# Performance work log

Hardware: AMD Instinct MI355X
Metric: run time of the kernel (lower is better)

## Reference

```python
import jax, jax.numpy as jnp
import numpy as np

B, N, D = 4, 8192, 128
H = 4 * D  # exp_factor * features
EPS = 1e-5


def layer_norm(x):
    # fresh nn.LayerNorm each call -> weight=1, bias=0 (no learned affine)
    mu = jnp.mean(x, axis=-1, keepdims=True)
    var = jnp.var(x, axis=-1, keepdims=True)
    return (x - mu) * jax.lax.rsqrt(var + EPS)


def setup_inputs() -> dict:
    key = jax.random.key(0)
    ks = jax.random.split(key, 8)
    x = jax.random.normal(ks[0], (B, N, D), dtype=jnp.float32)
    adj = jax.random.uniform(ks[1], (N, N), dtype=jnp.float32)
    attn_mask = jnp.ones((1,), dtype=jnp.int32)  # unused (torch masked_fill result discarded)
    pad_mask = jnp.ones((1,), dtype=jnp.int32)   # unused
    # FFN params (torch Linear default init scale ~ 1/sqrt(fan_in))
    w1 = jax.random.normal(ks[2], (D, H), dtype=jnp.float32) / np.sqrt(D)
    b1 = jnp.zeros((H,), dtype=jnp.float32)
    w2 = jax.random.normal(ks[3], (H, D), dtype=jnp.float32) / np.sqrt(H)
    b2 = jnp.zeros((D,), dtype=jnp.float32)
    return {"x": x, "adj": adj, "attn_mask": attn_mask, "pad_mask": pad_mask,
            "w1": w1, "b1": b1, "w2": w2, "b2": b2, "dim": 128}


def reference(x, adj, attn_mask, pad_mask, w1, b1, w2, b2, dim):
    # Sublayer 0: x + InrAwaSA(LN(x))
    h = layer_norm(x)                               # [B,N,D]
    # adj is provided -> scores = dense adj, shared across batch.
    # NOTE: masks are no-ops in the source (masked_fill not in-place).
    prob = jax.nn.softmax(adj, axis=-1)             # [N,N]
    attn_out = jnp.einsum('nm,bmd->bnd', prob, h)   # [B,N,D]
    x1 = x + attn_out
    # Sublayer 1: x1 + FFN(LN(x1))
    h1 = layer_norm(x1)
    ffn = jnp.maximum(h1 @ w1 + b1, 0.0) @ w2 + b2
    return x1 + ffn
```

## Files before the change

kernel.cpp:

```cpp
#include <hip/hip_runtime.h>
#include <hip/hip_bf16.h>

typedef __attribute__((ext_vector_type(8))) short bh8;
typedef __attribute__((ext_vector_type(4))) float fx4;
typedef __attribute__((ext_vector_type(8))) int i32x8;
typedef __attribute__((ext_vector_type(4))) int i32x4;

typedef const __attribute__((address_space(1))) unsigned int* gas_p;
typedef __attribute__((address_space(3))) unsigned int* las_p;

#define MFMA(a, b, c) __builtin_amdgcn_mfma_f32_16x16x32_bf16((a), (b), (c), 0, 0, 0)
#define MFMAS(a, b, c) __builtin_amdgcn_mfma_scale_f32_16x16x128_f8f6f4( \
    (a), (b), (c), 0, 0, 0, 0x7f7f7f7f, 0, 0x7f7f7f7f)

__device__ __forceinline__ unsigned short f2bf(float f) {
  unsigned u = __builtin_bit_cast(unsigned, f);
  u += 0x7fff + ((u >> 16) & 1);
  return (unsigned short)(u >> 16);
}

__device__ __forceinline__ float bflo2f(unsigned u) { return __builtin_bit_cast(float, u << 16); }

__device__ __forceinline__ void gld16(const void* g, void* l) {
  __builtin_amdgcn_global_load_lds((gas_p)g, (las_p)l, 16, 0, 0);
}

__global__ __launch_bounds__(256) void transpose_weights(const float* __restrict__ w1,
                                                         const float* __restrict__ w2,
                                                         unsigned short* __restrict__ w1t,
                                                         unsigned short* __restrict__ w2t) {
  const int tgl = blockIdx.x * 256 + threadIdx.x;
  { const int h = tgl >> 7, d = tgl & 127; w1t[tgl] = f2bf(w1[d * 512 + h]); }
  { const int d = tgl >> 9, h = tgl & 511; w2t[tgl] = f2bf(w2[h * 128 + d]); }
}

__global__ __launch_bounds__(256) void ln1_transpose(const float* __restrict__ x,
                                                     unsigned char* __restrict__ htf) {
  const int t = threadIdx.x, lane = t & 63, w = t >> 6;
  const int mt = blockIdx.x, b = blockIdx.y;
  __shared__ unsigned short tile[128 * 64];
  const float* xb = x + ((size_t)b * 8192 + (size_t)mt * 64) * 128;
  for (int it = 0; it < 16; ++it) {
    const int r = w * 16 + it;
    const float2 v = *(const float2*)(xb + r * 128 + lane * 2);
    float s = v.x + v.y, s2 = v.x * v.x + v.y * v.y;
    #pragma unroll
    for (int o = 1; o < 64; o <<= 1) { s += __shfl_xor(s, o); s2 += __shfl_xor(s2, o); }
    const float mean = s * 0.0078125f;
    const float var = s2 * 0.0078125f - mean * mean;
    const float rstd = rsqrtf(var + 1e-5f);
    const int mc = r >> 3, ml = r & 7;
    const int d0 = lane * 2, d1 = d0 + 1;
    tile[d0 * 64 + ((mc ^ (d0 & 7)) << 3) + ml] = f2bf((v.x - mean) * rstd);
    tile[d1 * 64 + ((mc ^ (d1 & 7)) << 3) + ml] = f2bf((v.y - mean) * rstd);
  }
  __syncthreads();
  #pragma unroll
  for (int i = 0; i < 4; ++i) {
    const int idx = i * 256 + t;
    const int d = idx >> 3, mc = idx & 7;
    const bh8 vv = *(const bh8*)(tile + d * 64 + ((mc ^ (d & 7)) << 3));
    int lo = 0, hi = 0;
    lo = __builtin_amdgcn_cvt_pk_fp8_f32(bflo2f((unsigned short)vv[0]),
                                         bflo2f((unsigned short)vv[1]), lo, false);
    lo = __builtin_amdgcn_cvt_pk_fp8_f32(bflo2f((unsigned short)vv[2]),
                                         bflo2f((unsigned short)vv[3]), lo, true);
    hi = __builtin_amdgcn_cvt_pk_fp8_f32(bflo2f((unsigned short)vv[4]),
                                         bflo2f((unsigned short)vv[5]), hi, false);
    hi = __builtin_amdgcn_cvt_pk_fp8_f32(bflo2f((unsigned short)vv[6]),
                                         bflo2f((unsigned short)vv[7]), hi, true);
    const int col = b * 128 + d;
    const int k0 = mt * 64 + mc * 8;
    const int frag = (k0 >> 7) * 32 + (col >> 4);
    const int off = ((col & 15) + 16 * ((k0 >> 5) & 3)) * 32 + (k0 & 31);
    *(uint2*)(htf + (size_t)frag * 2048 + off) = (uint2){(unsigned)lo, (unsigned)hi};
  }
}

__global__ __launch_bounds__(256) void softmax_frag(const float* __restrict__ adj,
                                                    unsigned char* __restrict__ probf) {
  const int t = threadIdx.x, lane = t & 63, w = t >> 6;
  const size_t n = blockIdx.x;
  __shared__ float red[4];
  __shared__ unsigned char sp[8192];
  const fx4* row = (const fx4*)(adj + n * 8192);
  fx4 v[8];
  float lsum = 0.f;
  #pragma unroll
  for (int i = 0; i < 8; ++i) {
    const fx4 a = row[i * 256 + t];
    fx4 e;
    e.x = __expf(a.x); e.y = __expf(a.y); e.z = __expf(a.z); e.w = __expf(a.w);
    v[i] = e;
    lsum += e.x + e.y + e.z + e.w;
  }
  #pragma unroll
  for (int o = 1; o < 64; o <<= 1) lsum += __shfl_xor(lsum, o);
  if (lane == 0) red[w] = lsum;
  __syncthreads();
  const float rinv = 4096.f / (red[0] + red[1] + red[2] + red[3]);
  #pragma unroll
  for (int i = 0; i < 8; ++i) {
    int pk = 0;
    pk = __builtin_amdgcn_cvt_pk_fp8_f32(v[i].x * rinv, v[i].y * rinv, pk, false);
    pk = __builtin_amdgcn_cvt_pk_fp8_f32(v[i].z * rinv, v[i].w * rinv, pk, true);
    const int g = 64 * i + (t >> 2);
    const int pg = g ^ ((g >> 4) & 7);
    *(unsigned*)&sp[pg * 16 + (t & 3) * 4] = (unsigned)pk;
  }
  __syncthreads();
  const int g0 = 2 * t, g1 = 2 * t + 1;
  const i32x4 q0 = *(const i32x4*)&sp[(g0 ^ ((g0 >> 4) & 7)) * 16];
  const i32x4 q1 = *(const i32x4*)&sp[(g1 ^ ((g1 >> 4) & 7)) * 16];
  unsigned char* dst = probf + (((n >> 4) * 64 + (t >> 2)) * 2048)
                     + (((int)(n & 15) + 16 * (t & 3)) * 32);
  *(i32x4*)dst = q0;
  *(i32x4*)(dst + 16) = q1;
}

__global__ __launch_bounds__(256, 2) void attn_gemm(const unsigned char* __restrict__ probf,
                                                    const unsigned char* __restrict__ htf,
                                                    unsigned short* __restrict__ pbuf) {
  const int tid = threadIdx.x, lane = tid & 63, wn = tid >> 6;
  const int mt = blockIdx.x, z = blockIdx.y;

  fx4 acc[4][8];
  #pragma unroll
  for (int i = 0; i < 4; ++i)
    #pragma unroll
    for (int j = 0; j < 8; ++j) acc[i][j] = (fx4){0.f, 0.f, 0.f, 0.f};

  for (int tt = 0; tt < 16; ++tt) {
    const int gkt = z * 16 + tt;
    i32x8 afr[4];
    #pragma unroll
    for (int mf = 0; mf < 4; ++mf) {
      const unsigned char* ap =
          probf + ((size_t)((mt * 4 + mf) * 64 + gkt)) * 2048 + lane * 32;
      const i32x4 lo = *(const i32x4*)ap;
      const i32x4 hi = *(const i32x4*)(ap + 16);
      afr[mf] = (i32x8){lo.x, lo.y, lo.z, lo.w, hi.x, hi.y, hi.z, hi.w};
    }
    const unsigned char* fb = htf + ((size_t)gkt * 32 + wn * 8) * 2048 + lane * 32;
    #pragma unroll
    for (int nf = 0; nf < 8; ++nf) {
      const i32x4 blo = *(const i32x4*)(fb + nf * 2048);
      const i32x4 bhi = *(const i32x4*)(fb + nf * 2048 + 16);
      const i32x8 bfr = (i32x8){blo.x, blo.y, blo.z, blo.w, bhi.x, bhi.y, bhi.z, bhi.w};
      #pragma unroll
      for (int mf = 0; mf < 4; ++mf)
        acc[mf][nf] = MFMAS(afr[mf], bfr, acc[mf][nf]);
    }
  }

  const float ds = 0.000244140625f;
  unsigned short* po = pbuf + (size_t)z * 8192 * 512;
  #pragma unroll
  for (int mf = 0; mf < 4; ++mf)
    #pragma unroll
    for (int nf = 0; nf < 8; ++nf) {
      const int col = wn * 128 + nf * 16 + (lane & 15);
      #pragma unroll
      for (int q = 0; q < 4; ++q) {
        const int row = mt * 64 + mf * 16 + (lane >> 4) * 4 + q;
        po[(size_t)row * 512 + col] = f2bf(acc[mf][nf][q] * ds);
      }
    }
}

#define SWZ16(ks, r) (((((ks) & 7) ^ ((r) & 7)) | ((ks) & 8)))
__global__ __launch_bounds__(512) void ln_ffn_kernel(const float* __restrict__ x,
                                                     const unsigned short* __restrict__ pbuf,
                                                     const unsigned short* __restrict__ w1t,
                                                     const unsigned short* __restrict__ w2t,
                                                     const float* __restrict__ b1,
                                                     const float* __restrict__ b2,
                                                     float* __restrict__ out) {
  const int t = threadIdx.x, lane = t & 63, w = t >> 6;
  const int wr = w >> 1, wc = w & 1;
  const int row0 = blockIdx.x * 128;
  __shared__ unsigned short As[128 * 128];
  __shared__ unsigned short W1c[128 * 128];
  __shared__ unsigned short W2c[128 * 128];
  __shared__ unsigned short Ts[128 * 128];

  auto stageW1 = [&](int hc) {
    #pragma unroll
    for (int i = 0; i < 4; ++i) {
      const int idx = i * 512 + t;
      const int row = idx >> 4, kc = idx & 15;
      const int kcs = (kc & 8) | ((kc & 7) ^ (row & 7));
      gld16(w1t + (size_t)(hc * 128 + row) * 128 + kcs * 8, W1c + (idx & ~63) * 8);
    }
  };
  auto stageW2 = [&](int hc) {
    #pragma unroll
    for (int i = 0; i < 4; ++i) {
      const int idx = i * 512 + t;
      const int row = idx >> 4, kc = idx & 15;
      const int kcs = (kc & 8) | ((kc & 7) ^ (row & 7));
      gld16(w2t + (size_t)row * 512 + hc * 128 + kcs * 8, W2c + (idx & ~63) * 8);
    }
  };

  stageW1(0); stageW2(0);

  const int r = t >> 2, q = t & 3, c0 = q * 32;
  const int rowg = row0 + r;
  const int bb = rowg >> 13, nn = rowg & 8191;
  float xv[32];
  {
    const float* xp = x + (size_t)rowg * 128 + c0;
    #pragma unroll
    for (int j = 0; j < 8; ++j) {
      const float4 v4 = *(const float4*)(xp + 4 * j);
      xv[4 * j] = v4.x; xv[4 * j + 1] = v4.y; xv[4 * j + 2] = v4.z; xv[4 * j + 3] = v4.w;
    }
    #pragma unroll
    for (int z = 0; z < 4; ++z) {
      const unsigned short* pp = pbuf + ((size_t)z * 8192 + nn) * 512 + bb * 128 + c0;
      #pragma unroll
      for (int j = 0; j < 4; ++j) {
        const bh8 pv = *(const bh8*)(pp + 8 * j);
        #pragma unroll
        for (int e = 0; e < 8; ++e) xv[8 * j + e] += bflo2f((unsigned short)pv[e]);
      }
    }
  }
  float s = 0.f, s2 = 0.f;
  #pragma unroll
  for (int j = 0; j < 32; ++j) { s += xv[j]; s2 += xv[j] * xv[j]; }
  s += __shfl_xor(s, 1); s2 += __shfl_xor(s2, 1);
  s += __shfl_xor(s, 2); s2 += __shfl_xor(s2, 2);
  const float mean = s * 0.0078125f;
  const float var = s2 * 0.0078125f - mean * mean;
  const float rstd = rsqrtf(var + 1e-5f);
  #pragma unroll
  for (int j = 0; j < 4; ++j) {
    const int g = q * 4 + j;
    bh8 pk;
    #pragma unroll
    for (int e = 0; e < 8; ++e) pk[e] = (short)f2bf((xv[8 * j + e] - mean) * rstd);
    *(bh8*)(As + r * 128 + SWZ16(g, r) * 8) = pk;
  }
  __syncthreads();

  fx4 accO[2][4];
  #pragma unroll
  for (int i = 0; i < 2; ++i)
    #pragma unroll
    for (int j = 0; j < 4; ++j) accO[i][j] = (fx4){0.f, 0.f, 0.f, 0.f};

  for (int hc = 0; hc < 4; ++hc) {
    if (hc > 0) stageW2(hc);
    fx4 accT[2][4];
    #pragma unroll
    for (int i = 0; i < 2; ++i)
      #pragma unroll
      for (int j = 0; j < 4; ++j) accT[i][j] = (fx4){0.f, 0.f, 0.f, 0.f};
    #pragma unroll
    for (int kk = 0; kk < 4; ++kk) {
      const int ks = kk * 4 + (lane >> 4);
      bh8 af[2], bfr[4];
      #pragma unroll
      for (int f = 0; f < 2; ++f) {
        const int ra = wr * 32 + f * 16 + (lane & 15);
        af[f] = *(const bh8*)(As + ra * 128 + SWZ16(ks, ra) * 8);
      }
      #pragma unroll
      for (int f = 0; f < 4; ++f) {
        const int rb = wc * 64 + f * 16 + (lane & 15);
        bfr[f] = *(const bh8*)(W1c + rb * 128 + SWZ16(ks, rb) * 8);
      }
      #pragma unroll
      for (int fm = 0; fm < 2; ++fm)
        #pragma unroll
        for (int fn = 0; fn < 4; ++fn) accT[fm][fn] = MFMA(af[fm], bfr[fn], accT[fm][fn]);
    }
    #pragma unroll
    for (int fm = 0; fm < 2; ++fm)
      #pragma unroll
      for (int fn = 0; fn < 4; ++fn) {
        const int col = wc * 64 + fn * 16 + (lane & 15);
        const float bv = b1[hc * 128 + col];
        const int c = col >> 3;
        #pragma unroll
        for (int qq = 0; qq < 4; ++qq) {
          const int row = wr * 32 + fm * 16 + (lane >> 4) * 4 + qq;
          float vv = accT[fm][fn][qq] + bv;
          vv = fmaxf(vv, 0.f);
          Ts[row * 128 + SWZ16(c, row) * 8 + (col & 7)] = f2bf(vv);
        }
      }
    __syncthreads();
    if (hc < 3) {
      stageW1(hc + 1);
    } else {
      float* dst = (r < 64) ? (float*)As + r * 128 + c0 : (float*)W1c + (r - 64) * 128 + c0;
      #pragma unroll
      for (int j = 0; j < 8; ++j)
        *(float4*)(dst + 4 * j) =
            (float4){xv[4 * j], xv[4 * j + 1], xv[4 * j + 2], xv[4 * j + 3]};
    }
    #pragma unroll
    for (int kk = 0; kk < 4; ++kk) {
      const int ks = kk * 4 + (lane >> 4);
      bh8 af[2], bfr[4];
      #pragma unroll
      for (int f = 0; f < 2; ++f) {
        const int ra = wr * 32 + f * 16 + (lane & 15);
        af[f] = *(const bh8*)(Ts + ra * 128 + SWZ16(ks, ra) * 8);
      }
      #pragma unroll
      for (int f = 0; f < 4; ++f) {
        const int rb = wc * 64 + f * 16 + (lane & 15);
        bfr[f] = *(const bh8*)(W2c + rb * 128 + SWZ16(ks, rb) * 8);
      }
      #pragma unroll
      for (int fm = 0; fm < 2; ++fm)
        #pragma unroll
        for (int fn = 0; fn < 4; ++fn) accO[fm][fn] = MFMA(af[fm], bfr[fn], accO[fm][fn]);
    }
    __syncthreads();
  }

  const float* x1a = (const float*)As;
  const float* x1b = (const float*)W1c;
  float* op = out + (size_t)row0 * 128;
  #pragma unroll
  for (int fm = 0; fm < 2; ++fm)
    #pragma unroll
    for (int fn = 0; fn < 4; ++fn) {
      const int col = wc * 64 + fn * 16 + (lane & 15);
      const float bv = b2[col];
      #pragma unroll
      for (int qq = 0; qq < 4; ++qq) {
        const int row = wr * 32 + fm * 16 + (lane >> 4) * 4 + qq;
        const float x1v = (row < 64) ? x1a[row * 128 + col] : x1b[(row - 64) * 128 + col];
        op[row * 128 + col] = x1v + accO[fm][fn][qq] + bv;
      }
    }
}

extern "C" void kernel_launch(void* const* d_in, const int* in_sizes, int n_in,
                              void* d_out, int out_size, void* d_ws, size_t ws_size,
                              hipStream_t stream) {
  const float* x   = (const float*)d_in[0];
  const float* adj = (const float*)d_in[1];
  const float* w1  = (const float*)d_in[4];
  const float* b1  = (const float*)d_in[5];
  const float* w2  = (const float*)d_in[6];
  const float* b2  = (const float*)d_in[7];
  float* out = (float*)d_out;

  char* p = (char*)d_ws;
  unsigned short* w1t  = (unsigned short*)p; p += (size_t)512 * 128 * 2;
  unsigned short* w2t  = (unsigned short*)p; p += (size_t)128 * 512 * 2;
  unsigned char*  htf  = (unsigned char*)p;  p += (size_t)4 * 128 * 8192;
  unsigned short* pbuf = (unsigned short*)p; p += (size_t)4 * 8192 * 512 * 2;
  unsigned char*  probf = (unsigned char*)p; p += (size_t)8192 * 8192;

  transpose_weights<<<256, 256, 0, stream>>>(w1, w2, w1t, w2t);
  ln1_transpose<<<dim3(128, 4), 256, 0, stream>>>(x, htf);
  softmax_frag<<<8192, 256, 0, stream>>>(adj, probf);
  attn_gemm<<<dim3(128, 4), 256, 0, stream>>>(probf, htf, pbuf);
  ln_ffn_kernel<<<256, 512, 0, stream>>>(x, pbuf, w1t, w2t, b1, b2, out);
}
```

Measured before the change: 186.0 us.

## Store softmax probabilities row-major and read MFMA fragments directly in GEMM

The softmax kernel now writes FP8 probabilities in plain row-major order with coalesced stores, dropping the LDS staging, the extra barrier and the swizzled fragment layout. The attention GEMM computes per-lane row pointers and loads its A fragments straight from the row-major matrix. This makes the softmax pass cheaper, but each GEMM lane now reads 32 bytes from a different row 8 KB apart, which could hurt coalescing and cache behaviour in the dominant GEMM.

```diff
diff --git a/kernel.cpp b/kernel.cpp
--- a/kernel.cpp
+++ b/kernel.cpp
@@ -77,13 +77,12 @@
   }
 }
 
-__global__ __launch_bounds__(256) void softmax_frag(const float* __restrict__ adj,
-                                                    unsigned char* __restrict__ probf) {
+__global__ __launch_bounds__(256) void softmax_rows(const float* __restrict__ adj,
+                                                    unsigned char* __restrict__ prob) {
   const int t = threadIdx.x, lane = t & 63, w = t >> 6;
-  const size_t n = blockIdx.x;
+  const size_t r = blockIdx.x;
   __shared__ float red[4];
-  __shared__ unsigned char sp[8192];
-  const fx4* row = (const fx4*)(adj + n * 8192);
+  const fx4* row = (const fx4*)(adj + r * 8192);
   fx4 v[8];
   float lsum = 0.f;
   #pragma unroll
@@ -99,26 +98,17 @@
   if (lane == 0) red[w] = lsum;
   __syncthreads();
   const float rinv = 4096.f / (red[0] + red[1] + red[2] + red[3]);
+  unsigned* po = (unsigned*)(prob + r * 8192);
   #pragma unroll
   for (int i = 0; i < 8; ++i) {
     int pk = 0;
     pk = __builtin_amdgcn_cvt_pk_fp8_f32(v[i].x * rinv, v[i].y * rinv, pk, false);
     pk = __builtin_amdgcn_cvt_pk_fp8_f32(v[i].z * rinv, v[i].w * rinv, pk, true);
-    const int g = 64 * i + (t >> 2);
-    const int pg = g ^ ((g >> 4) & 7);
-    *(unsigned*)&sp[pg * 16 + (t & 3) * 4] = (unsigned)pk;
-  }
-  __syncthreads();
-  const int g0 = 2 * t, g1 = 2 * t + 1;
-  const i32x4 q0 = *(const i32x4*)&sp[(g0 ^ ((g0 >> 4) & 7)) * 16];
-  const i32x4 q1 = *(const i32x4*)&sp[(g1 ^ ((g1 >> 4) & 7)) * 16];
-  unsigned char* dst = probf + (((n >> 4) * 64 + (t >> 2)) * 2048)
-                     + (((int)(n & 15) + 16 * (t & 3)) * 32);
-  *(i32x4*)dst = q0;
-  *(i32x4*)(dst + 16) = q1;
-}
-
-__global__ __launch_bounds__(256, 2) void attn_gemm(const unsigned char* __restrict__ probf,
+    po[i * 256 + t] = (unsigned)pk;
+  }
+}
+
+__global__ __launch_bounds__(256, 2) void attn_gemm(const unsigned char* __restrict__ prob,
                                                     const unsigned char* __restrict__ htf,
                                                     unsigned short* __restrict__ pbuf) {
   const int tid = threadIdx.x, lane = tid & 63, wn = tid >> 6;
@@ -130,13 +120,18 @@
     #pragma unroll
     for (int j = 0; j < 8; ++j) acc[i][j] = (fx4){0.f, 0.f, 0.f, 0.f};
 
+  const unsigned char* arow[4];
+  #pragma unroll
+  for (int mf = 0; mf < 4; ++mf)
+    arow[mf] = prob + (size_t)(mt * 64 + mf * 16 + (lane & 15)) * 8192 + (lane >> 4) * 32;
+
   for (int tt = 0; tt < 16; ++tt) {
     const int gkt = z * 16 + tt;
+    const size_t ko = (size_t)gkt * 128;
     i32x8 afr[4];
     #pragma unroll
     for (int mf = 0; mf < 4; ++mf) {
-      const unsigned char* ap =
-          probf + ((size_t)((mt * 4 + mf) * 64 + gkt)) * 2048 + lane * 32;
+      const unsigned char* ap = arow[mf] + ko;
       const i32x4 lo = *(const i32x4*)ap;
       const i32x4 hi = *(const i32x4*)(ap + 16);
       afr[mf] = (i32x8){lo.x, lo.y, lo.z, lo.w, hi.x, hi.y, hi.z, hi.w};
@@ -358,11 +353,11 @@
   unsigned short* w2t  = (unsigned short*)p; p += (size_t)128 * 512 * 2;
   unsigned char*  htf  = (unsigned char*)p;  p += (size_t)4 * 128 * 8192;
   unsigned short* pbuf = (unsigned short*)p; p += (size_t)4 * 8192 * 512 * 2;
-  unsigned char*  probf = (unsigned char*)p; p += (size_t)8192 * 8192;
+  unsigned char*  prob = (unsigned char*)p;  p += (size_t)8192 * 8192;
 
   transpose_weights<<<256, 256, 0, stream>>>(w1, w2, w1t, w2t);
   ln1_transpose<<<dim3(128, 4), 256, 0, stream>>>(x, htf);
-  softmax_frag<<<8192, 256, 0, stream>>>(adj, probf);
-  attn_gemm<<<dim3(128, 4), 256, 0, stream>>>(probf, htf, pbuf);
+  softmax_rows<<<8192, 256, 0, stream>>>(adj, prob);
+  attn_gemm<<<dim3(128, 4), 256, 0, stream>>>(prob, htf, pbuf);
   ln_ffn_kernel<<<256, 512, 0, stream>>>(x, pbuf, w1t, w2t, b1, b2, out);
 }
```

After: 176.1 us. 1.06x faster.
